# Optimization experiments

Hardware: AMD Instinct MI355X
Metric: run time of the kernel (lower is better)

The kernel has to match this reference:

```python
import jax, jax.numpy as jnp
import numpy as np

B, V, H = 4, 256, 128
EPS = 1e-5


def setup_inputs() -> dict:
    key = jax.random.key(0)
    ks = jax.random.split(key, 16)
    s = 1.0 / np.sqrt(H)
    d = {}
    d["h"] = jax.random.normal(ks[0], (B, V, H), jnp.float32)
    d["e"] = jax.random.normal(ks[1], (B, V, V, H), jnp.float32)
    d["A"] = jax.random.bernoulli(ks[2], 0.5, (B, V, V))
    d["S"] = jax.random.bernoulli(ks[3], 0.5, (B, V, V))
    for i, n in enumerate("UVABC"):
        d["W" + n] = (jax.random.normal(ks[4 + i], (H, H), jnp.float32) * s)
        d["b" + n] = jnp.zeros((H,), jnp.float32)
    d["gamma_h"] = jnp.ones((H,), jnp.float32)
    d["beta_h"] = jnp.zeros((H,), jnp.float32)
    d["gamma_e"] = jnp.ones((H,), jnp.float32)
    d["beta_e"] = jnp.zeros((H,), jnp.float32)
    return d


def _batchnorm(x2d, gamma, beta):
    # BatchNorm1d with batch statistics (track_running_stats=False), biased var
    m = x2d.mean(axis=0)
    v = x2d.var(axis=0)
    return (x2d - m) * jax.lax.rsqrt(v + EPS) * gamma + beta


def reference(h, e, A, S, WU, bU, WV, bV, WA, bA, WB, bB, WC, bC,
              gamma_h, beta_h, gamma_e, beta_e):
    b, v, hd = h.shape
    h_in, e_in = h, e

    Uh = h @ WU.T + bU                      # (B,V,H)
    Vh = h @ WV.T + bV                      # (B,V,H)
    Ah = h @ WA.T + bA
    Bh = h @ WB.T + bB
    Ce = e @ WC.T + bC                      # (B,V,V,H)

    # e_new[b,i,j] = Ah[b,j] + Bh[b,i] + Ce[b,i,j]
    e_new = Ah[:, None, :, :] + Bh[:, :, None, :] + Ce
    gates = jax.nn.sigmoid(e_new)

    # aggregate(Vh, S, gates): zero where S is True, then sum over j
    Vh_b = Vh[:, None, :, :]                # (B,1,V,H) -> neighbor j features
    agg_S = jnp.sum(jnp.where(S[..., None], 0.0, gates * Vh_b), axis=2)
    # aggregate(Vh, A, gates=1): sum_j (1 - A[i,j]) * Vh[j] as a matmul
    agg_A = jnp.einsum('bij,bjh->bih', (~A).astype(Vh.dtype), Vh)

    h_new = Uh + agg_S + agg_A

    h_new = _batchnorm(h_new.reshape(b * v, hd), gamma_h, beta_h).reshape(b, v, hd)
    e_new = _batchnorm(e_new.reshape(b * v * v, hd), gamma_e, beta_e).reshape(b, v, v, hd)

    h_out = h_in + jax.nn.relu(h_new)
    e_out = e_in + jax.nn.relu(e_new)
    return (h_out, e_out)
```

## Files before the change

kernel.cpp:

```cpp
#include <hip/hip_runtime.h>

#define BB 4
#define VV 256
#define HH 128
#define NROWS (BB*VV)
#define NE_CNT (BB*VV*VV)
#define EPSV 1e-5f

typedef float4 f4;

__device__ __forceinline__ float sigm(float x) {
    return 1.f / (1.f + __expf(-x));
}

__global__ __launch_bounds__(256) void k_linear4(
    const float* __restrict__ h,
    const float* __restrict__ W0, const float* __restrict__ b0,
    const float* __restrict__ W1, const float* __restrict__ b1,
    const float* __restrict__ W2, const float* __restrict__ b2,
    const float* __restrict__ W3, const float* __restrict__ b3,
    float* __restrict__ out)
{
    __shared__ float hs[4*HH];
    const int tid = threadIdx.x;
    const int r0  = blockIdx.x * 4;
    if (tid < 128) {
        int r = tid >> 5, kq = (tid & 31) << 2;
        *(f4*)&hs[r*HH + kq] = *(const f4*)&h[(r0 + r)*HH + kq];
    }
    __syncthreads();
    const int n  = tid & 127;
    const int s0 = tid >> 7;
    const float* Ws[4] = {W0, W1, W2, W3};
    const float* bs[4] = {b0, b1, b2, b3};
    for (int ss = 0; ss < 2; ++ss) {
        const int sel = s0 + ss*2;
        const float* wrow = Ws[sel] + n*HH;
        float a0=0.f, a1=0.f, a2=0.f, a3=0.f;
        for (int kq = 0; kq < 32; ++kq) {
            f4 w = *(const f4*)&wrow[kq<<2];
            float wq[4] = {w.x, w.y, w.z, w.w};
            #pragma unroll
            for (int q = 0; q < 4; ++q) {
                int k = (kq<<2) + q;
                float wv = wq[q];
                a0 += hs[0*HH + k] * wv;
                a1 += hs[1*HH + k] * wv;
                a2 += hs[2*HH + k] * wv;
                a3 += hs[3*HH + k] * wv;
            }
        }
        float bias = bs[sel][n];
        float* o = out + sel*(NROWS*HH);
        o[(r0+0)*HH + n] = a0 + bias;
        o[(r0+1)*HH + n] = a1 + bias;
        o[(r0+2)*HH + n] = a2 + bias;
        o[(r0+3)*HH + n] = a3 + bias;
    }
}

__global__ __launch_bounds__(256) void k_transpose(
    const float* __restrict__ in, float* __restrict__ out)
{
    __shared__ float t[32][33];
    int ti = blockIdx.x >> 2, tj = blockIdx.x & 3;
    int tx = threadIdx.x & 31, ty = threadIdx.x >> 5;
    for (int yy = ty; yy < 32; yy += 8)
        t[yy][tx] = in[(ti*32 + yy)*HH + tj*32 + tx];
    __syncthreads();
    for (int yy = ty; yy < 32; yy += 8)
        out[(tj*32 + yy)*HH + ti*32 + tx] = t[tx][yy];
}

__global__ __launch_bounds__(256, 2) void k_edge(
    const float* __restrict__ e, const int* __restrict__ A, const int* __restrict__ S,
    const float* __restrict__ WCt, const float* __restrict__ bC,
    const float* __restrict__ Ahw, const float* __restrict__ Bhw,
    const float* __restrict__ Vhw,
    float* __restrict__ eout, float* __restrict__ aggS, float* __restrict__ aggA,
    float* __restrict__ sums)
{
    __shared__ float es[256*36];
    __shared__ float wc[32*132];
    __shared__ float s_aggS[HH], s_aggA[HH], s_sum[HH], s_ssq[HH];

    const int t  = threadIdx.x;
    const int bi = blockIdx.x;
    const int b  = bi >> 8;
    if (t < HH) { s_aggS[t]=0.f; s_aggA[t]=0.f; s_sum[t]=0.f; s_ssq[t]=0.f; }

    const int tn  = t & 7;
    const int tjg = t >> 3;

    float acc[8][16];
    #pragma unroll
    for (int jj = 0; jj < 8; ++jj)
        #pragma unroll
        for (int q = 0; q < 16; ++q) acc[jj][q] = 0.f;

    const f4* e4   = (const f4*)e;
    const f4* wct4 = (const f4*)WCt;

    for (int kc = 0; kc < 4; ++kc) {
        __syncthreads();
        #pragma unroll
        for (int m = 0; m < 8; ++m) {
            int idx = m*256 + t;
            int j = idx >> 3, kq = idx & 7;
            *(f4*)&es[j*36 + kq*4] = e4[(bi*VV + j)*32 + kc*8 + kq];
        }
        #pragma unroll
        for (int m = 0; m < 4; ++m) {
            int idx = m*256 + t;
            int k = idx >> 5, n4 = idx & 31;
            *(f4*)&wc[k*132 + n4*4] = wct4[(kc*32 + k)*32 + n4];
        }
        __syncthreads();
        #pragma unroll
        for (int kq = 0; kq < 8; ++kq) {
            f4 aj[8];
            #pragma unroll
            for (int jj = 0; jj < 8; ++jj)
                aj[jj] = *(const f4*)&es[(tjg + jj*32)*36 + kq*4];
            #pragma unroll
            for (int kk = 0; kk < 4; ++kk) {
                f4 wq[4];
                #pragma unroll
                for (int q = 0; q < 4; ++q)
                    wq[q] = *(const f4*)&wc[(kq*4 + kk)*132 + tn*4 + q*32];
                #pragma unroll
                for (int jj = 0; jj < 8; ++jj) {
                    float a = (kk==0) ? aj[jj].x : (kk==1) ? aj[jj].y
                            : (kk==2) ? aj[jj].z : aj[jj].w;
                    #pragma unroll
                    for (int q = 0; q < 4; ++q) {
                        acc[jj][q*4+0] += a*wq[q].x;
                        acc[jj][q*4+1] += a*wq[q].y;
                        acc[jj][q*4+2] += a*wq[q].z;
                        acc[jj][q*4+3] += a*wq[q].w;
                    }
                }
            }
        }
    }

    float bcv[16], bhv[16];
    #pragma unroll
    for (int q = 0; q < 4; ++q) {
        f4 bc4 = *(const f4*)&bC[tn*4 + q*32];
        f4 bh4 = *(const f4*)&Bhw[bi*HH + tn*4 + q*32];
        bcv[q*4+0]=bc4.x; bcv[q*4+1]=bc4.y; bcv[q*4+2]=bc4.z; bcv[q*4+3]=bc4.w;
        bhv[q*4+0]=bh4.x; bhv[q*4+1]=bh4.y; bhv[q*4+2]=bh4.z; bhv[q*4+3]=bh4.w;
    }
    float sm[16], sq[16], aS[16], aA[16];
    #pragma unroll
    for (int q = 0; q < 16; ++q) { sm[q]=0.f; sq[q]=0.f; aS[q]=0.f; aA[q]=0.f; }

    const int* Sp = S + bi*VV;
    const int* Ap = A + bi*VV;
    #pragma unroll
    for (int jj = 0; jj < 8; ++jj) {
        const int j = tjg + jj*32;
        const float* ahp = &Ahw[(b*VV + j)*HH];
        const float* vhp = &Vhw[(b*VV + j)*HH];
        const int Sij = Sp[j], Aij = Ap[j];
        #pragma unroll
        for (int q = 0; q < 4; ++q) {
            f4 ah = *(const f4*)&ahp[tn*4 + q*32];
            f4 vh = *(const f4*)&vhp[tn*4 + q*32];
            f4 env;
            env.x = acc[jj][q*4+0] + bcv[q*4+0] + bhv[q*4+0] + ah.x;
            env.y = acc[jj][q*4+1] + bcv[q*4+1] + bhv[q*4+1] + ah.y;
            env.z = acc[jj][q*4+2] + bcv[q*4+2] + bhv[q*4+2] + ah.z;
            env.w = acc[jj][q*4+3] + bcv[q*4+3] + bhv[q*4+3] + ah.w;
            *(f4*)&eout[((size_t)(bi*VV) + j)*HH + tn*4 + q*32] = env;
            float vv[4] = {vh.x, vh.y, vh.z, vh.w};
            float ev[4] = {env.x, env.y, env.z, env.w};
            #pragma unroll
            for (int qq = 0; qq < 4; ++qq) {
                float v = ev[qq];
                sm[q*4+qq] += v;
                sq[q*4+qq] += v*v;
                if (!Aij) aA[q*4+qq] += vv[qq];
                if (!Sij) aS[q*4+qq] += vv[qq] * sigm(v);
            }
        }
    }
    #pragma unroll
    for (int q = 0; q < 4; ++q)
        #pragma unroll
        for (int qq = 0; qq < 4; ++qq) {
            int n = tn*4 + q*32 + qq;
            atomicAdd(&s_sum[n],  sm[q*4+qq]);
            atomicAdd(&s_ssq[n],  sq[q*4+qq]);
            atomicAdd(&s_aggS[n], aS[q*4+qq]);
            atomicAdd(&s_aggA[n], aA[q*4+qq]);
        }
    __syncthreads();
    if (t < HH) {
        aggS[bi*HH + t] = s_aggS[t];
        aggA[bi*HH + t] = s_aggA[t];
        atomicAdd(&sums[t],      s_sum[t]);
        atomicAdd(&sums[HH + t], s_ssq[t]);
    }
}

__global__ __launch_bounds__(256) void k_hnew(
    const float* __restrict__ Uh, const float* __restrict__ aggS,
    const float* __restrict__ aggA, float* __restrict__ h_new,
    float* __restrict__ sums)
{
    __shared__ float ssm[HH], ssq[HH];
    const int tid = threadIdx.x;
    if (tid < 128) { ssm[tid]=0.f; ssq[tid]=0.f; }
    __syncthreads();
    int gid = blockIdx.x*256 + tid;
    f4 u = *(const f4*)&Uh[gid*4];
    f4 s = *(const f4*)&aggS[gid*4];
    f4 a = *(const f4*)&aggA[gid*4];
    float v0=u.x+s.x+a.x, v1=u.y+s.y+a.y, v2=u.z+s.z+a.z, v3=u.w+s.w+a.w;
    *(f4*)&h_new[gid*4] = make_float4(v0,v1,v2,v3);
    int n0 = (gid*4) & 127;
    atomicAdd(&ssm[n0+0], v0); atomicAdd(&ssq[n0+0], v0*v0);
    atomicAdd(&ssm[n0+1], v1); atomicAdd(&ssq[n0+1], v1*v1);
    atomicAdd(&ssm[n0+2], v2); atomicAdd(&ssq[n0+2], v2*v2);
    atomicAdd(&ssm[n0+3], v3); atomicAdd(&ssq[n0+3], v3*v3);
    __syncthreads();
    if (tid < 128) {
        atomicAdd(&sums[256 + tid], ssm[tid]);
        atomicAdd(&sums[384 + tid], ssq[tid]);
    }
}

__global__ void k_stats(const float* __restrict__ sums, float* __restrict__ outs,
                        const float* __restrict__ gamma_e, const float* __restrict__ beta_e,
                        const float* __restrict__ gamma_h, const float* __restrict__ beta_h)
{
    int n = threadIdx.x;
    float em  = sums[n] * (1.f/(float)NE_CNT);
    float ev  = sums[128+n] * (1.f/(float)NE_CNT) - em*em;
    float esc = rsqrtf(ev + EPSV) * gamma_e[n];
    outs[n]       = esc;
    outs[128 + n] = beta_e[n] - em*esc;
    float hm  = sums[256+n] * (1.f/1024.f);
    float hv  = sums[384+n] * (1.f/1024.f) - hm*hm;
    float hsc = rsqrtf(hv + EPSV) * gamma_h[n];
    outs[256 + n] = hsc;
    outs[384 + n] = beta_h[n] - hm*hsc;
}

__global__ __launch_bounds__(256) void k_hout(
    const float* __restrict__ h_in, const float* __restrict__ h_new,
    const float* __restrict__ outs, float* __restrict__ hout)
{
    int gid = blockIdx.x*256 + threadIdx.x;
    int n0 = (gid*4) & 127;
    f4 x  = *(const f4*)&h_new[gid*4];
    f4 hi = *(const f4*)&h_in[gid*4];
    f4 sc = *(const f4*)&outs[256 + n0];
    f4 sh = *(const f4*)&outs[384 + n0];
    f4 y;
    y.x = fmaxf(x.x*sc.x + sh.x, 0.f) + hi.x;
    y.y = fmaxf(x.y*sc.y + sh.y, 0.f) + hi.y;
    y.z = fmaxf(x.z*sc.z + sh.z, 0.f) + hi.z;
    y.w = fmaxf(x.w*sc.w + sh.w, 0.f) + hi.w;
    *(f4*)&hout[gid*4] = y;
}

__global__ __launch_bounds__(256) void k_eout(
    const float* __restrict__ e_in, const float* __restrict__ outs,
    float* __restrict__ eio)
{
    size_t gid = (size_t)blockIdx.x*256 + threadIdx.x;
    int n0 = ((int)(gid & 31)) << 2;
    f4 x  = *(const f4*)&eio[gid*4];
    f4 ei = *(const f4*)&e_in[gid*4];
    f4 sc = *(const f4*)&outs[n0];
    f4 sh = *(const f4*)&outs[128 + n0];
    f4 y;
    y.x = fmaxf(x.x*sc.x + sh.x, 0.f) + ei.x;
    y.y = fmaxf(x.y*sc.y + sh.y, 0.f) + ei.y;
    y.z = fmaxf(x.z*sc.z + sh.z, 0.f) + ei.z;
    y.w = fmaxf(x.w*sc.w + sh.w, 0.f) + ei.w;
    *(f4*)&eio[gid*4] = y;
}

extern "C" void kernel_launch(void* const* d_in, const int* in_sizes, int n_in,
                              void* d_out, int out_size, void* d_ws, size_t ws_size,
                              hipStream_t stream)
{
    (void)in_sizes; (void)n_in; (void)out_size; (void)ws_size;
    const float* h   = (const float*)d_in[0];
    const float* e   = (const float*)d_in[1];
    const int*   A   = (const int*)d_in[2];
    const int*   S   = (const int*)d_in[3];
    const float* WU  = (const float*)d_in[4];   const float* bU = (const float*)d_in[5];
    const float* WV  = (const float*)d_in[6];   const float* bV = (const float*)d_in[7];
    const float* WA_ = (const float*)d_in[8];   const float* bA = (const float*)d_in[9];
    const float* WB_ = (const float*)d_in[10];  const float* bB = (const float*)d_in[11];
    const float* WC_ = (const float*)d_in[12];  const float* bC = (const float*)d_in[13];
    const float* gamma_h = (const float*)d_in[14]; const float* beta_h = (const float*)d_in[15];
    const float* gamma_e = (const float*)d_in[16]; const float* beta_e = (const float*)d_in[17];

    float* ws    = (float*)d_ws;
    float* Uh    = ws;
    float* Vh    = ws + 131072;
    float* Ahw   = ws + 262144;
    float* Bhw   = ws + 393216;
    float* aggS  = ws + 524288;
    float* aggA  = ws + 655360;
    float* h_new = ws + 786432;
    float* WCt   = ws + 917504;
    float* sums  = ws + 933888;
    float* outs  = ws + 934400;

    float* hout = (float*)d_out;
    float* eout = (float*)d_out + NROWS*HH;

    hipMemsetAsync(sums, 0, 512*sizeof(float), stream);
    k_linear4 <<<256,   256, 0, stream>>>(h, WU,bU, WV,bV, WA_,bA, WB_,bB, Uh);
    k_transpose<<<16,   256, 0, stream>>>(WC_, WCt);
    k_edge    <<<1024,  256, 0, stream>>>(e, A, S, WCt, bC, Ahw, Bhw, Vh,
                                          eout, aggS, aggA, sums);
    k_hnew    <<<128,   256, 0, stream>>>(Uh, aggS, aggA, h_new, sums);
    k_stats   <<<1,     128, 0, stream>>>(sums, outs, gamma_e, beta_e, gamma_h, beta_h);
    k_hout    <<<128,   256, 0, stream>>>(h, h_new, outs, hout);
    k_eout    <<<32768, 256, 0, stream>>>(e, outs, eout);
}
```

Before: 543.3 us.

## Double-buffer edge GEMM with register prefetch, swizzled LDS, 512-thread blocks

Restructures the fused edge-projection kernel. Blocks now have 512 threads, each computing an 8x8 output tile instead of 8x16, which lowers register pressure and raises occupancy. The k-dimension is split into 8 chunks of 16 held in double-buffered shared memory, and the next chunk is prefetched into registers while the current one is computed, so one barrier per chunk replaces two. An XOR swizzle on the e tile replaces padding to avoid LDS bank conflicts. The risks are more global load instructions per byte and a more complex index mapping.

Result: slower. 1.798 ms (+230.9%).

```diff
diff --git a/kernel.cpp b/kernel.cpp
--- a/kernel.cpp
+++ b/kernel.cpp
@@ -12,6 +12,8 @@
 __device__ __forceinline__ float sigm(float x) {
     return 1.f / (1.f + __expf(-x));
 }
+
+#define COMP(v,kk) ((kk)==0 ? (v).x : (kk)==1 ? (v).y : (kk)==2 ? (v).z : (v).w)
 
 __global__ __launch_bounds__(256) void k_linear4(
     const float* __restrict__ h,
@@ -72,7 +74,7 @@
         out[(tj*32 + yy)*HH + ti*32 + tx] = t[tx][yy];
 }
 
-__global__ __launch_bounds__(256, 2) void k_edge(
+__global__ __launch_bounds__(512, 4) void k_edge(
     const float* __restrict__ e, const int* __restrict__ A, const int* __restrict__ S,
     const float* __restrict__ WCt, const float* __restrict__ bC,
     const float* __restrict__ Ahw, const float* __restrict__ Bhw,
@@ -80,8 +82,8 @@
     float* __restrict__ eout, float* __restrict__ aggS, float* __restrict__ aggA,
     float* __restrict__ sums)
 {
-    __shared__ float es[256*36];
-    __shared__ float wc[32*132];
+    __shared__ float es[2][4096];
+    __shared__ float wc[2][2048];
     __shared__ float s_aggS[HH], s_aggA[HH], s_sum[HH], s_ssq[HH];
 
     const int t  = threadIdx.x;
@@ -89,91 +91,101 @@
     const int b  = bi >> 8;
     if (t < HH) { s_aggS[t]=0.f; s_aggA[t]=0.f; s_sum[t]=0.f; s_ssq[t]=0.f; }
 
-    const int tn  = t & 7;
-    const int tjg = t >> 3;
-
-    float acc[8][16];
+    const int tn  = t & 15;
+    const int tjg = t >> 4;
+
+    float acc[8][8];
     #pragma unroll
     for (int jj = 0; jj < 8; ++jj)
         #pragma unroll
-        for (int q = 0; q < 16; ++q) acc[jj][q] = 0.f;
+        for (int q = 0; q < 8; ++q) acc[jj][q] = 0.f;
 
     const f4* e4   = (const f4*)e;
     const f4* wct4 = (const f4*)WCt;
 
-    for (int kc = 0; kc < 4; ++kc) {
+    const int j0 = t >> 2;
+    const int sp = (t & 3) ^ (j0 & 3);
+    const f4* p_es0 = e4 + (size_t)(bi*VV + j0)*32 + sp;
+    const f4* p_es1 = p_es0 + (size_t)128*32;
+    const f4* p_wc  = wct4 + t;
+
+    f4 r0 = p_es0[0];
+    f4 r1 = p_es1[0];
+    f4 rw = p_wc[0];
+
+    #pragma unroll 2
+    for (int kc = 0; kc < 8; ++kc) {
+        float* esb = es[kc & 1];
+        float* wcb = wc[kc & 1];
+        *(f4*)&esb[t*4]        = r0;
+        *(f4*)&esb[2048 + t*4] = r1;
+        *(f4*)&wcb[t*4]        = rw;
         __syncthreads();
+        if (kc < 7) {
+            r0 = p_es0[(kc+1)*4];
+            r1 = p_es1[(kc+1)*4];
+            rw = p_wc[(kc+1)*512];
+        }
         #pragma unroll
-        for (int m = 0; m < 8; ++m) {
-            int idx = m*256 + t;
-            int j = idx >> 3, kq = idx & 7;
-            *(f4*)&es[j*36 + kq*4] = e4[(bi*VV + j)*32 + kc*8 + kq];
-        }
-        #pragma unroll
-        for (int m = 0; m < 4; ++m) {
-            int idx = m*256 + t;
-            int k = idx >> 5, n4 = idx & 31;
-            *(f4*)&wc[k*132 + n4*4] = wct4[(kc*32 + k)*32 + n4];
-        }
-        __syncthreads();
-        #pragma unroll
-        for (int kq = 0; kq < 8; ++kq) {
-            f4 aj[8];
+        for (int kq = 0; kq < 4; ++kq) {
+            const int sw = ((kq ^ (tjg & 3)) << 2);
             #pragma unroll
-            for (int jj = 0; jj < 8; ++jj)
-                aj[jj] = *(const f4*)&es[(tjg + jj*32)*36 + kq*4];
-            #pragma unroll
-            for (int kk = 0; kk < 4; ++kk) {
-                f4 wq[4];
+            for (int jh = 0; jh < 2; ++jh) {
+                f4 a0 = *(const f4*)&esb[(tjg + (jh*4+0)*32)*16 + sw];
+                f4 a1 = *(const f4*)&esb[(tjg + (jh*4+1)*32)*16 + sw];
+                f4 a2 = *(const f4*)&esb[(tjg + (jh*4+2)*32)*16 + sw];
+                f4 a3 = *(const f4*)&esb[(tjg + (jh*4+3)*32)*16 + sw];
                 #pragma unroll
-                for (int q = 0; q < 4; ++q)
-                    wq[q] = *(const f4*)&wc[(kq*4 + kk)*132 + tn*4 + q*32];
-                #pragma unroll
-                for (int jj = 0; jj < 8; ++jj) {
-                    float a = (kk==0) ? aj[jj].x : (kk==1) ? aj[jj].y
-                            : (kk==2) ? aj[jj].z : aj[jj].w;
+                for (int kk = 0; kk < 4; ++kk) {
+                    const float* wrow = &wcb[(kq*4 + kk)*128 + tn*4];
+                    f4 w0 = *(const f4*)&wrow[0];
+                    f4 w1 = *(const f4*)&wrow[64];
+                    float v0 = COMP(a0,kk), v1 = COMP(a1,kk);
+                    float v2 = COMP(a2,kk), v3 = COMP(a3,kk);
                     #pragma unroll
-                    for (int q = 0; q < 4; ++q) {
-                        acc[jj][q*4+0] += a*wq[q].x;
-                        acc[jj][q*4+1] += a*wq[q].y;
-                        acc[jj][q*4+2] += a*wq[q].z;
-                        acc[jj][q*4+3] += a*wq[q].w;
+                    for (int jl = 0; jl < 4; ++jl) {
+                        float a = (jl==0)?v0:(jl==1)?v1:(jl==2)?v2:v3;
+                        float* ac = acc[jh*4 + jl];
+                        ac[0] += a*w0.x; ac[1] += a*w0.y;
+                        ac[2] += a*w0.z; ac[3] += a*w0.w;
+                        ac[4] += a*w1.x; ac[5] += a*w1.y;
+                        ac[6] += a*w1.z; ac[7] += a*w1.w;
                     }
                 }
             }
         }
     }
 
-    float bcv[16], bhv[16];
-    #pragma unroll
-    for (int q = 0; q < 4; ++q) {
-        f4 bc4 = *(const f4*)&bC[tn*4 + q*32];
-        f4 bh4 = *(const f4*)&Bhw[bi*HH + tn*4 + q*32];
+    float bcv[8], bhv[8];
+    #pragma unroll
+    for (int q = 0; q < 2; ++q) {
+        f4 bc4 = *(const f4*)&bC[tn*4 + q*64];
+        f4 bh4 = *(const f4*)&Bhw[bi*HH + tn*4 + q*64];
         bcv[q*4+0]=bc4.x; bcv[q*4+1]=bc4.y; bcv[q*4+2]=bc4.z; bcv[q*4+3]=bc4.w;
         bhv[q*4+0]=bh4.x; bhv[q*4+1]=bh4.y; bhv[q*4+2]=bh4.z; bhv[q*4+3]=bh4.w;
     }
-    float sm[16], sq[16], aS[16], aA[16];
-    #pragma unroll
-    for (int q = 0; q < 16; ++q) { sm[q]=0.f; sq[q]=0.f; aS[q]=0.f; aA[q]=0.f; }
+    float sm[8], sq[8], aS[8], aA[8];
+    #pragma unroll
+    for (int q = 0; q < 8; ++q) { sm[q]=0.f; sq[q]=0.f; aS[q]=0.f; aA[q]=0.f; }
 
     const int* Sp = S + bi*VV;
     const int* Ap = A + bi*VV;
     #pragma unroll
     for (int jj = 0; jj < 8; ++jj) {
         const int j = tjg + jj*32;
-        const float* ahp = &Ahw[(b*VV + j)*HH];
-        const float* vhp = &Vhw[(b*VV + j)*HH];
+        const float* ahp = &Ahw[(size_t)(b*VV + j)*HH];
+        const float* vhp = &Vhw[(size_t)(b*VV + j)*HH];
         const int Sij = Sp[j], Aij = Ap[j];
         #pragma unroll
-        for (int q = 0; q < 4; ++q) {
-            f4 ah = *(const f4*)&ahp[tn*4 + q*32];
-            f4 vh = *(const f4*)&vhp[tn*4 + q*32];
+        for (int q = 0; q < 2; ++q) {
+            f4 ah = *(const f4*)&ahp[tn*4 + q*64];
+            f4 vh = *(const f4*)&vhp[tn*4 + q*64];
             f4 env;
             env.x = acc[jj][q*4+0] + bcv[q*4+0] + bhv[q*4+0] + ah.x;
             env.y = acc[jj][q*4+1] + bcv[q*4+1] + bhv[q*4+1] + ah.y;
             env.z = acc[jj][q*4+2] + bcv[q*4+2] + bhv[q*4+2] + ah.z;
             env.w = acc[jj][q*4+3] + bcv[q*4+3] + bhv[q*4+3] + ah.w;
-            *(f4*)&eout[((size_t)(bi*VV) + j)*HH + tn*4 + q*32] = env;
+            *(f4*)&eout[((size_t)(bi*VV) + j)*HH + tn*4 + q*64] = env;
             float vv[4] = {vh.x, vh.y, vh.z, vh.w};
             float ev[4] = {env.x, env.y, env.z, env.w};
             #pragma unroll
@@ -187,10 +199,10 @@
         }
     }
     #pragma unroll
-    for (int q = 0; q < 4; ++q)
+    for (int q = 0; q < 2; ++q)
         #pragma unroll
         for (int qq = 0; qq < 4; ++qq) {
-            int n = tn*4 + q*32 + qq;
+            int n = tn*4 + q*64 + qq;
             atomicAdd(&s_sum[n],  sm[q*4+qq]);
             atomicAdd(&s_ssq[n],  sq[q*4+qq]);
             atomicAdd(&s_aggS[n], aS[q*4+qq]);
@@ -320,7 +332,7 @@
     hipMemsetAsync(sums, 0, 512*sizeof(float), stream);
     k_linear4 <<<256,   256, 0, stream>>>(h, WU,bU, WV,bV, WA_,bA, WB_,bB, Uh);
     k_transpose<<<16,   256, 0, stream>>>(WC_, WCt);
-    k_edge    <<<1024,  256, 0, stream>>>(e, A, S, WCt, bC, Ahw, Bhw, Vh,
+    k_edge    <<<1024,  512, 0, stream>>>(e, A, S, WCt, bC, Ahw, Bhw, Vh,
                                           eout, aggS, aggA, sums);
     k_hnew    <<<128,   256, 0, stream>>>(Uh, aggS, aggA, h_new, sums);
     k_stats   <<<1,     128, 0, stream>>>(sums, outs, gamma_e, beta_e, gamma_h, beta_h);
```
